# Kernel optimization log

Hardware: AMD Instinct MI355X
Metric: run time of the kernel (lower is better)

Reference implementation:

```python
import jax, jax.numpy as jnp
import numpy as np

N_NODES = 100000


def _gcn_norm(edge_index, edge_weight, n):
    # add self-loops with weight 1 (PyG gcn_norm default fill_value=1.0)
    row = jnp.concatenate([edge_index[0], jnp.arange(n, dtype=edge_index.dtype)])
    col = jnp.concatenate([edge_index[1], jnp.arange(n, dtype=edge_index.dtype)])
    w = jnp.concatenate([edge_weight, jnp.ones((n,), dtype=edge_weight.dtype)])
    deg = jax.ops.segment_sum(w, col, num_segments=n)
    dinv = jnp.where(deg > 0, jax.lax.rsqrt(jnp.where(deg > 0, deg, 1.0)), 0.0)
    norm = dinv[row] * w * dinv[col]  # [E+N]
    return row, col, norm


def _gcn_conv(x, row, col, norm, W, b, n):
    h = x @ W                                   # [N, out] dense projection first (in > out)
    msg = norm[:, None] * h[row]                # gather + scale
    out = jax.ops.segment_sum(msg, col, num_segments=n)  # scatter-add to targets
    return out + b


def setup_inputs() -> dict:
    key = jax.random.key(0)
    ks = jax.random.split(key, 6)
    n, e, f, h, c = N_NODES, 3200000, 256, 64, 40
    return {
        "x": jax.random.normal(ks[0], (n, f), dtype=jnp.float32),
        "edge_index": jax.random.randint(ks[1], (2, e), 0, n, dtype=jnp.int64),
        "edge_weight": jax.random.uniform(ks[2], (e,), dtype=jnp.float32),
        "W1": jax.random.normal(ks[3], (f, h), dtype=jnp.float32) / np.sqrt(f),
        "b1": jnp.zeros((h,), dtype=jnp.float32),
        "W2": jax.random.normal(ks[4], (h, c), dtype=jnp.float32) / np.sqrt(h),
        "b2": jnp.zeros((c,), dtype=jnp.float32),
    }


def reference(x, edge_index, edge_weight, W1, b1, W2, b2):
    n = x.shape[0]
    row, col, norm = _gcn_norm(edge_index, edge_weight, n)
    # layer 1: GCNConv -> identity activation -> dropout (identity at eval)
    h = _gcn_conv(x, row, col, norm, W1, b1, n)
    # layer 2: GCNConv (classifier head)
    out = _gcn_conv(h, row, col, norm, W2, b2, n)
    return out
```

## Files before the change

kernel.cpp:

```cpp
#include <hip/hip_runtime.h>
#include <hip/hip_fp16.h>
#include <cstdint>
#include <cstddef>


#define TB 256
#define NBK 200
#define LCAP 32
#define SPLIT 4
#define GCAP 2048
#define NSL 8

typedef _Float16 half8 __attribute__((ext_vector_type(8)));
typedef float f32x4 __attribute__((ext_vector_type(4)));

__global__ void k_detect(const unsigned* ei, int* flag) {
    int t = threadIdx.x;
    unsigned v = 0;
    for (int i = t; i < 256; i += 64) v |= ei[2 * i + 1];
    unsigned long long any = __ballot(v != 0u);
    if (t == 0) *flag = (any != 0ull) ? 1 : 0;
}

__global__ void k_zero(int* p, int n) {
    int i = blockIdx.x * blockDim.x + threadIdx.x;
    if (i < n) p[i] = 0;
}

__global__ __launch_bounds__(256) void k_binA(const void* __restrict__ ei,
                                              const int* __restrict__ flag,
                                              const float* __restrict__ ew,
                                              int* __restrict__ tail,
                                              int2* __restrict__ stage,
                                              int per, int E, int capx) {
    __shared__ int2 lbuf[NBK][LCAP];
    __shared__ int lcnt[NBK];
    int t = threadIdx.x;
    int myx = blockIdx.x & (NSL - 1);
    for (int i = t; i < NBK; i += 256) lcnt[i] = 0;
    __syncthreads();
    int s0 = blockIdx.x * per;
    int s1 = min(E, s0 + per);
    int isI32 = *flag;
    const int* p32 = (const int*)ei;
    const long long* p64 = (const long long*)ei;
    for (int b0 = s0; b0 < s1; b0 += 2048) {
        int2 ent[8];
        int bk[8];
#pragma unroll
        for (int u = 0; u < 8; u++) {
            int e = b0 + u * 256 + t;
            bk[u] = -1;
            if (e < s1) {
                int r, c;
                if (isI32) { r = p32[e]; c = p32[E + e]; }
                else       { r = (int)p64[e]; c = (int)p64[E + e]; }
                bk[u] = c >> 9;
                ent[u] = make_int2((r << 9) | (c & 511), __float_as_int(ew[e]));
            }
        }
#pragma unroll
        for (int u = 0; u < 8; u++) {
            if (bk[u] < 0) continue;
            int pos = atomicAdd(&lcnt[bk[u]], 1);
            if (pos < LCAP) {
                lbuf[bk[u]][pos] = ent[u];
            } else {
                int slot = bk[u] * NSL + myx;
                int g = atomicAdd(&tail[slot], 1);
                if (g < capx) stage[(size_t)slot * capx + g] = ent[u];
            }
        }
        __syncthreads();
        if (t < NBK) {
            int c = min(lcnt[t], LCAP);
            int n16 = c & ~15;
            if (n16) {
                int slot = t * NSL + myx;
                int base = atomicAdd(&tail[slot], n16);
                size_t db = (size_t)slot * capx;
                for (int j = 0; j < n16; j++) {
                    int g = base + j;
                    if (g < capx) stage[db + g] = lbuf[t][j];
                }
                int rem = c - n16;
                for (int j = 0; j < rem; j++) lbuf[t][j] = lbuf[t][n16 + j];
                lcnt[t] = rem;
            } else {
                lcnt[t] = c;
            }
        }
        __syncthreads();
    }
    if (t < NBK) {
        int c = min(lcnt[t], LCAP);
        if (c) {
            int slot = t * NSL + myx;
            int base = atomicAdd(&tail[slot], c);
            size_t db = (size_t)slot * capx;
            for (int j = 0; j < c; j++) {
                int g = base + j;
                if (g < capx) stage[db + g] = lbuf[t][j];
            }
        }
    }
}

__global__ void k_bscan(const int* __restrict__ tail, int* __restrict__ bbase,
                        int* __restrict__ ptr2, int nbk, int capx, int N) {
    __shared__ int sm[256];
    int t = threadIdx.x;
    int v = 0;
    if (t < nbk)
        for (int x = 0; x < NSL; x++) v += min(tail[t * NSL + x], capx);
    sm[t] = v;
    __syncthreads();
    for (int off = 1; off < 256; off <<= 1) {
        int add = (t >= off) ? sm[t - off] : 0;
        __syncthreads();
        sm[t] += add;
        __syncthreads();
    }
    if (t < nbk) bbase[t] = sm[t] - v;
    if (t == nbk - 1) ptr2[(size_t)N * 4] = sm[t];
}

__global__ __launch_bounds__(512) void k_binB(const int* __restrict__ tail,
                                              const int* __restrict__ bbase,
                                              const int2* __restrict__ stage,
                                              int2* __restrict__ csr,
                                              int* __restrict__ ptr2,
                                              float* __restrict__ dinv,
                                              int N, int capx, int qn) {
    __shared__ int h2[2048];
    __shared__ float wsm[512];
    __shared__ int sm[512];
    __shared__ int lpos2[2048];
    __shared__ int cseg[NSL];
    int b = blockIdx.x, t = threadIdx.x;
    for (int i = t; i < 2048; i += 512) h2[i] = 0;
    wsm[t] = 0.f;
    if (t < NSL) cseg[t] = min(tail[b * NSL + t], capx);
    __syncthreads();
#pragma unroll
    for (int x = 0; x < NSL; x++) {
        int m = cseg[x];
        size_t sb = (size_t)(b * NSL + x) * capx;
        for (int j = t; j < m; j += 512) {
            int2 v = stage[sb + j];
            int cl = v.x & 511;
            int src = v.x >> 9;
            int rng = min(src / qn, SPLIT - 1);
            atomicAdd(&h2[(cl << 2) | rng], 1);
            atomicAdd(&wsm[cl], __int_as_float(v.y));
        }
    }
    __syncthreads();
    int a0 = h2[t * 4], a1 = h2[t * 4 + 1], a2 = h2[t * 4 + 2], a3 = h2[t * 4 + 3];
    int s = a0 + a1 + a2 + a3;
    sm[t] = s;
    __syncthreads();
    for (int off = 1; off < 512; off <<= 1) {
        int add = (t >= off) ? sm[t - off] : 0;
        __syncthreads();
        sm[t] += add;
        __syncthreads();
    }
    int ex = sm[t] - s;
    int base = bbase[b];
    int node = b * 512 + t;
    int e0 = ex, e1 = ex + a0, e2 = e1 + a1, e3 = e2 + a2;
    float dv = rsqrtf(1.0f + wsm[t]);
    if (node < N) {
        ptr2[(size_t)node * 4 + 0] = base + e0;
        ptr2[(size_t)node * 4 + 1] = base + e1;
        ptr2[(size_t)node * 4 + 2] = base + e2;
        ptr2[(size_t)node * 4 + 3] = base + e3;
        dinv[node] = dv;
    }
    lpos2[t * 4 + 0] = e0;
    lpos2[t * 4 + 1] = e1;
    lpos2[t * 4 + 2] = e2;
    lpos2[t * 4 + 3] = e3;
    __syncthreads();
    wsm[t] = dv;
    __syncthreads();
#pragma unroll
    for (int x = 0; x < NSL; x++) {
        int m = cseg[x];
        size_t sb = (size_t)(b * NSL + x) * capx;
        for (int j = t; j < m; j += 512) {
            int2 v = stage[sb + j];
            int cl = v.x & 511;
            int src = v.x >> 9;
            int rng = min(src / qn, SPLIT - 1);
            int idx = atomicAdd(&lpos2[(cl << 2) | rng], 1);
            float wfold = __int_as_float(v.y) * wsm[cl];
            csr[base + idx] = make_int2(src, __float_as_int(wfold));
        }
    }
}

__global__ void k_fold(int2* __restrict__ csr, const float* __restrict__ dinv,
                       const int* __restrict__ ptr2, int n4) {
    int tot = ptr2[n4];
    int j = blockIdx.x * blockDim.x + threadIdx.x;
    if (j >= tot) return;
    int2 e = csr[j];
    csr[j].y = __float_as_int(__int_as_float(e.y) * dinv[e.x]);
}

__global__ void k_wc(const float* __restrict__ W1, const float* __restrict__ b1,
                     const float* __restrict__ W2, __half* __restrict__ Wcf,
                     float* __restrict__ bw) {
    __shared__ float w2s[64 * 40];
    __shared__ __half wcs[256][40];
    int t = threadIdx.x;
    for (int i = t; i < 64 * 40; i += 256) w2s[i] = W2[i];
    __syncthreads();
    float acc[40];
#pragma unroll
    for (int j = 0; j < 40; j++) acc[j] = 0.f;
    for (int k = 0; k < 64; k++) {
        float a = W1[t * 64 + k];
#pragma unroll
        for (int j = 0; j < 40; j++) acc[j] = fmaf(a, w2s[k * 40 + j], acc[j]);
    }
    for (int j = 0; j < 40; j++) wcs[t][j] = __float2half(acc[j]);
    if (t < 40) {
        float accb = 0.f;
        for (int k = 0; k < 64; k++) accb = fmaf(b1[k], w2s[k * 40 + t], accb);
        bw[t] = accb;
    }
    __syncthreads();
    for (int s = 0; s < 48; s++) {
        int o = t * 48 + s;
        int j = o & 7;
        int lane = (o >> 3) & 63;
        int f = o >> 9;
        int nt = f % 3, kt = f / 3;
        int k = kt * 32 + (lane >> 4) * 8 + j;
        int c = nt * 16 + (lane & 15);
        Wcf[o] = (c < 40) ? wcs[k][c] : __float2half(0.f);
    }
}

__global__ __launch_bounds__(256, 2) void k_zmm(const float* __restrict__ x,
                                                const __half* __restrict__ Wcf,
                                                __half* __restrict__ Zh, int n) {
    __shared__ __align__(16) unsigned char xs[128 * 64 * 2];
    int t = threadIdx.x;
    int w = t >> 6;
    int l = t & 63;
    int rlo = l & 15;
    int khi = l >> 4;
    int row0 = blockIdx.x * 128;
    f32x4 acc[2][3];
#pragma unroll
    for (int m = 0; m < 2; m++)
#pragma unroll
        for (int nt = 0; nt < 3; nt++) acc[m][nt] = (f32x4){0.f, 0.f, 0.f, 0.f};

    for (int k0 = 0; k0 < 256; k0 += 64) {
        __syncthreads();
#pragma unroll
        for (int s = 0; s < 8; s++) {
            int i = t + 256 * s;
            int rr = i >> 4;
            int kq = (i & 15) * 4;
            int grow = min(row0 + rr, n - 1);
            float4 v = *(const float4*)&x[(size_t)grow * 256 + k0 + kq];
            __half2 h01 = __floats2half2_rn(v.x, v.y);
            __half2 h23 = __floats2half2_rn(v.z, v.w);
            float2 pk;
            ((__half2*)&pk)[0] = h01;
            ((__half2*)&pk)[1] = h23;
            int byte = (rr * 128 + kq * 2) ^ ((rr & 7) << 4);
            *(float2*)(xs + byte) = pk;
        }
        __syncthreads();
        half8 bfr[2][3];
#pragma unroll
        for (int kt2 = 0; kt2 < 2; kt2++)
#pragma unroll
            for (int nt = 0; nt < 3; nt++) {
                int f = (k0 / 32 + kt2) * 3 + nt;
                bfr[kt2][nt] = *(const half8*)&Wcf[(size_t)(f * 64 + l) * 8];
            }
#pragma unroll
        for (int kt2 = 0; kt2 < 2; kt2++) {
#pragma unroll
            for (int m = 0; m < 2; m++) {
                int row = (w * 2 + m) * 16 + rlo;
                int byte = (row * 128 + kt2 * 64 + khi * 16) ^ ((row & 7) << 4);
                half8 af = *(const half8*)(xs + byte);
#pragma unroll
                for (int nt = 0; nt < 3; nt++)
                    acc[m][nt] = __builtin_amdgcn_mfma_f32_16x16x32_f16(af, bfr[kt2][nt], acc[m][nt], 0, 0, 0);
            }
        }
    }
#pragma unroll
    for (int m = 0; m < 2; m++) {
#pragma unroll
        for (int nt = 0; nt < 3; nt++) {
            int col = nt * 16 + rlo;
            if (col < 40) {
#pragma unroll
                for (int reg = 0; reg < 4; reg++) {
                    int grow = row0 + (w * 2 + m) * 16 + khi * 4 + reg;
                    if (grow < n) Zh[(size_t)grow * 40 + col] = __float2half(acc[m][nt][reg]);
                }
            }
        }
    }
}

template <int MODE>
__global__ __launch_bounds__(320) void k_gather(const int* __restrict__ ptr2,
                                                const int2* __restrict__ csr,
                                                const __half* __restrict__ src,
                                                const float* __restrict__ dinv,
                                                const float* __restrict__ bw,
                                                const float* __restrict__ b2,
                                                __half* __restrict__ dsth,
                                                float* __restrict__ dstf, int n) {
    __shared__ int2 se[GCAP];
    int t = threadIdx.x;
    int ln = t / 5;
    int q = t - ln * 5;
    int c0 = q * 8;
    int n0 = blockIdx.x * 64;
    int node = n0 + ln;
    int n1 = min(n0 + 64, n);
    int st0 = ptr2[(size_t)n0 * 4];
    int en0 = ptr2[(size_t)n1 * 4];
    bool act = (node < n1);
    float d2 = 0.f;
    int st = 0, en = 0;
    float a0 = 0.f, a1 = 0.f, a2 = 0.f, a3 = 0.f, a4 = 0.f, a5 = 0.f, a6 = 0.f, a7 = 0.f;
    float sw = 0.f;
    if (act) {
        float d = dinv[node];
        d2 = d * d;
        st = ptr2[(size_t)node * 4];
        en = ptr2[(size_t)(node + 1) * 4];
        float4 raw = *(const float4*)&src[(size_t)node * 40 + c0];
        const __half2* hh = (const __half2*)&raw;
        float2 f0 = __half22float2(hh[0]), f1 = __half22float2(hh[1]);
        float2 f2 = __half22float2(hh[2]), f3 = __half22float2(hh[3]);
        a0 = d2 * f0.x; a1 = d2 * f0.y; a2 = d2 * f1.x; a3 = d2 * f1.y;
        a4 = d2 * f2.x; a5 = d2 * f2.y; a6 = d2 * f3.x; a7 = d2 * f3.y;
    }
    for (int base = st0; base < en0; base += GCAP) {
        int m = min(GCAP, en0 - base);
        __syncthreads();
        for (int i = t; i < m; i += 320) se[i] = csr[base + i];
        __syncthreads();
        if (act) {
            int lo = max(st, base) - base;
            int hi = min(en, base + m) - base;
#pragma unroll 4
            for (int j = lo; j < hi; j++) {
                int2 e = se[j];
                float nv = __int_as_float(e.y);
                float4 raw = *(const float4*)&src[(size_t)e.x * 40 + c0];
                const __half2* hh = (const __half2*)&raw;
                float2 f0 = __half22float2(hh[0]), f1 = __half22float2(hh[1]);
                float2 f2 = __half22float2(hh[2]), f3 = __half22float2(hh[3]);
                if (MODE) sw += nv;
                a0 = fmaf(nv, f0.x, a0); a1 = fmaf(nv, f0.y, a1);
                a2 = fmaf(nv, f1.x, a2); a3 = fmaf(nv, f1.y, a3);
                a4 = fmaf(nv, f2.x, a4); a5 = fmaf(nv, f2.y, a5);
                a6 = fmaf(nv, f3.x, a6); a7 = fmaf(nv, f3.y, a7);
            }
        }
    }
    if (!act) return;
    if (MODE) {
        float sb = sw + d2;
        a0 += sb * bw[c0 + 0] + b2[c0 + 0];
        a1 += sb * bw[c0 + 1] + b2[c0 + 1];
        a2 += sb * bw[c0 + 2] + b2[c0 + 2];
        a3 += sb * bw[c0 + 3] + b2[c0 + 3];
        a4 += sb * bw[c0 + 4] + b2[c0 + 4];
        a5 += sb * bw[c0 + 5] + b2[c0 + 5];
        a6 += sb * bw[c0 + 6] + b2[c0 + 6];
        a7 += sb * bw[c0 + 7] + b2[c0 + 7];
        float4 o0 = make_float4(a0, a1, a2, a3);
        float4 o1 = make_float4(a4, a5, a6, a7);
        *(float4*)&dstf[(size_t)node * 40 + c0] = o0;
        *(float4*)&dstf[(size_t)node * 40 + c0 + 4] = o1;
    } else {
        float4 packed;
        ((__half2*)&packed)[0] = __floats2half2_rn(a0, a1);
        ((__half2*)&packed)[1] = __floats2half2_rn(a2, a3);
        ((__half2*)&packed)[2] = __floats2half2_rn(a4, a5);
        ((__half2*)&packed)[3] = __floats2half2_rn(a6, a7);
        *(float4*)&dsth[(size_t)node * 40 + c0] = packed;
    }
}

extern "C" void kernel_launch(void* const* d_in, const int* in_sizes, int n_in,
                              void* d_out, int out_size, void* d_ws, size_t ws_size,
                              hipStream_t stream) {
    const float* x  = (const float*)d_in[0];
    const void*  ei = d_in[1];
    const float* ew = (const float*)d_in[2];
    const float* W1 = (const float*)d_in[3];
    const float* b1 = (const float*)d_in[4];
    const float* W2 = (const float*)d_in[5];
    const float* b2 = (const float*)d_in[6];
    float* out = (float*)d_out;

    const int E = in_sizes[1] / 2;
    const int N = in_sizes[0] / 256;
    const int nbk = (N + 511) >> 9;
    const int capx = E / (nbk * NSL) + 768;
    const int qn = (N + SPLIT - 1) / SPLIT;

    char* ws = (char*)d_ws;
    float*  dinv = (float*)(ws + 0);
    int*    flag = (int*)(ws + (1u << 19));
    float*  bw   = (float*)(ws + (1u << 19) + 256);
    __half* Wcf  = (__half*)(ws + (1u << 19) + 4096);
    int*    tail = (int*)(ws + (1u << 19) + 65536);
    int*    bbase = (int*)(ws + (1u << 19) + 65536 + 16384);
    size_t off = (size_t)1 << 20;
    size_t estride = ((size_t)E * 4 + 255) & ~(size_t)255;
    size_t n4stride = ((size_t)(N * 4 + 1) * 4 + 255) & ~(size_t)255;
    size_t hstride = ((size_t)N * 40 * 2 + 255) & ~(size_t)255;
    int*    ptr2 = (int*)(ws + off);    off += n4stride;
    int2*   csr  = (int2*)(ws + off);   off += 2 * estride;
    int2*   stage = (int2*)(ws + off);  off += (size_t)NBK * NSL * capx * 8;
    __half* Zh   = (__half*)(ws + off); off += hstride;
    __half* T1h  = (__half*)(ws + off);

    const int NB = 608;
    const int per = (E + NB - 1) / NB;
    int gb = (N + 63) / 64;

    k_detect<<<1, 64, 0, stream>>>((const unsigned*)ei, flag);
    k_zero<<<(NBK * NSL + TB - 1) / TB, TB, 0, stream>>>(tail, NBK * NSL);
    k_binA<<<NB, 256, 0, stream>>>(ei, flag, ew, tail, stage, per, E, capx);
    k_bscan<<<1, 256, 0, stream>>>(tail, bbase, ptr2, nbk, capx, N);
    k_binB<<<nbk, 512, 0, stream>>>(tail, bbase, stage, csr, ptr2, dinv, N, capx, qn);
    k_fold<<<(E + TB - 1) / TB, TB, 0, stream>>>(csr, dinv, ptr2, N * 4);
    k_wc<<<1, TB, 0, stream>>>(W1, b1, W2, Wcf, bw);
    k_zmm<<<(N + 127) / 128, TB, 0, stream>>>(x, Wcf, Zh, N);
    k_gather<0><<<gb, 320, 0, stream>>>(ptr2, csr, Zh, dinv, bw, b2, T1h, nullptr, N);
    k_gather<1><<<gb, 320, 0, stream>>>(ptr2, csr, T1h, dinv, bw, b2, nullptr, out, N);
}
```

Baseline: 278.8 us.

## Split CSR binning into quarter-bucket blocks with LDS-staged coalesced writes

Each destination bucket of 512 nodes is now handled by four 256-thread blocks, one per 128-node quarter, which gives four times as many blocks for better GPU occupancy. Every block still scans the whole bucket's staged edges but only processes its own quarter. Per-quarter edge counts are reduced with wave shuffles to compute the output offset. Edges are scattered into an LDS buffer and then copied to the CSR array in coalesced order rather than scattered straight to global memory. The cost is reading the staged data four times, and edges beyond QCAP per quarter are silently dropped.

```diff
diff --git a/kernel.cpp b/kernel.cpp
--- a/kernel.cpp
+++ b/kernel.cpp
@@ -10,6 +10,7 @@
 #define SPLIT 4
 #define GCAP 2048
 #define NSL 8
+#define QCAP 5120
 
 typedef _Float16 half8 __attribute__((ext_vector_type(8)));
 typedef float f32x4 __attribute__((ext_vector_type(4)));
@@ -125,80 +126,106 @@
     if (t == nbk - 1) ptr2[(size_t)N * 4] = sm[t];
 }
 
-__global__ __launch_bounds__(512) void k_binB(const int* __restrict__ tail,
+__global__ __launch_bounds__(256) void k_binB(const int* __restrict__ tail,
                                               const int* __restrict__ bbase,
                                               const int2* __restrict__ stage,
                                               int2* __restrict__ csr,
                                               int* __restrict__ ptr2,
                                               float* __restrict__ dinv,
                                               int N, int capx, int qn) {
-    __shared__ int h2[2048];
-    __shared__ float wsm[512];
-    __shared__ int sm[512];
-    __shared__ int lpos2[2048];
+    __shared__ int2 lent[QCAP];
+    __shared__ int h2[512];
+    __shared__ int lpos[512];
+    __shared__ int sm[256];
+    __shared__ float wsm[128];
     __shared__ int cseg[NSL];
-    int b = blockIdx.x, t = threadIdx.x;
-    for (int i = t; i < 2048; i += 512) h2[i] = 0;
-    wsm[t] = 0.f;
+    __shared__ int qtot[4];
+    int b = blockIdx.x >> 2;
+    int qtr = blockIdx.x & 3;
+    int t = threadIdx.x;
+    for (int i = t; i < 512; i += 256) h2[i] = 0;
+    if (t < 128) wsm[t] = 0.f;
     if (t < NSL) cseg[t] = min(tail[b * NSL + t], capx);
-    __syncthreads();
-#pragma unroll
+    if (t < 4) qtot[t] = 0;
+    __syncthreads();
+    int cq0 = 0, cq1 = 0, cq2 = 0, cq3 = 0;
     for (int x = 0; x < NSL; x++) {
         int m = cseg[x];
         size_t sb = (size_t)(b * NSL + x) * capx;
-        for (int j = t; j < m; j += 512) {
+        for (int j = t; j < m; j += 256) {
             int2 v = stage[sb + j];
             int cl = v.x & 511;
-            int src = v.x >> 9;
-            int rng = min(src / qn, SPLIT - 1);
-            atomicAdd(&h2[(cl << 2) | rng], 1);
-            atomicAdd(&wsm[cl], __int_as_float(v.y));
-        }
-    }
-    __syncthreads();
-    int a0 = h2[t * 4], a1 = h2[t * 4 + 1], a2 = h2[t * 4 + 2], a3 = h2[t * 4 + 3];
-    int s = a0 + a1 + a2 + a3;
-    sm[t] = s;
-    __syncthreads();
-    for (int off = 1; off < 512; off <<= 1) {
+            int q = cl >> 7;
+            cq0 += (q == 0); cq1 += (q == 1); cq2 += (q == 2); cq3 += (q == 3);
+            if (q == qtr) {
+                int src = v.x >> 9;
+                int rng = min(src / qn, SPLIT - 1);
+                atomicAdd(&h2[((cl & 127) << 2) | rng], 1);
+                atomicAdd(&wsm[cl & 127], __int_as_float(v.y));
+            }
+        }
+    }
+#pragma unroll
+    for (int off = 32; off; off >>= 1) {
+        cq0 += __shfl_down(cq0, off);
+        cq1 += __shfl_down(cq1, off);
+        cq2 += __shfl_down(cq2, off);
+        cq3 += __shfl_down(cq3, off);
+    }
+    if ((t & 63) == 0) {
+        atomicAdd(&qtot[0], cq0);
+        atomicAdd(&qtot[1], cq1);
+        atomicAdd(&qtot[2], cq2);
+        atomicAdd(&qtot[3], cq3);
+    }
+    __syncthreads();
+    int p0 = h2[2 * t], p1 = h2[2 * t + 1];
+    int ps = p0 + p1;
+    sm[t] = ps;
+    __syncthreads();
+    for (int off = 1; off < 256; off <<= 1) {
         int add = (t >= off) ? sm[t - off] : 0;
         __syncthreads();
         sm[t] += add;
         __syncthreads();
     }
-    int ex = sm[t] - s;
-    int base = bbase[b];
-    int node = b * 512 + t;
-    int e0 = ex, e1 = ex + a0, e2 = e1 + a1, e3 = e2 + a2;
-    float dv = rsqrtf(1.0f + wsm[t]);
-    if (node < N) {
-        ptr2[(size_t)node * 4 + 0] = base + e0;
-        ptr2[(size_t)node * 4 + 1] = base + e1;
-        ptr2[(size_t)node * 4 + 2] = base + e2;
-        ptr2[(size_t)node * 4 + 3] = base + e3;
-        dinv[node] = dv;
-    }
-    lpos2[t * 4 + 0] = e0;
-    lpos2[t * 4 + 1] = e1;
-    lpos2[t * 4 + 2] = e2;
-    lpos2[t * 4 + 3] = e3;
-    __syncthreads();
-    wsm[t] = dv;
-    __syncthreads();
-#pragma unroll
+    int ex = sm[t] - ps;
+    int qb = bbase[b];
+    if (qtr > 0) qb += qtot[0];
+    if (qtr > 1) qb += qtot[1];
+    if (qtr > 2) qb += qtot[2];
+    lpos[2 * t] = ex;
+    lpos[2 * t + 1] = ex + p0;
+    int nodeBase = b * 512 + qtr * 128;
+    {
+        int k0 = 2 * t, k1 = 2 * t + 1;
+        int nl0 = nodeBase + (k0 >> 2), nl1 = nodeBase + (k1 >> 2);
+        if (nl0 < N) ptr2[(size_t)nl0 * 4 + (k0 & 3)] = qb + ex;
+        if (nl1 < N) ptr2[(size_t)nl1 * 4 + (k1 & 3)] = qb + ex + p0;
+    }
+    if (t < 128) {
+        float dv = rsqrtf(1.0f + wsm[t]);
+        if (nodeBase + t < N) dinv[nodeBase + t] = dv;
+        wsm[t] = dv;
+    }
+    __syncthreads();
     for (int x = 0; x < NSL; x++) {
         int m = cseg[x];
         size_t sb = (size_t)(b * NSL + x) * capx;
-        for (int j = t; j < m; j += 512) {
+        for (int j = t; j < m; j += 256) {
             int2 v = stage[sb + j];
             int cl = v.x & 511;
+            if ((cl >> 7) != qtr) continue;
             int src = v.x >> 9;
             int rng = min(src / qn, SPLIT - 1);
-            int idx = atomicAdd(&lpos2[(cl << 2) | rng], 1);
-            float wfold = __int_as_float(v.y) * wsm[cl];
-            csr[base + idx] = make_int2(src, __float_as_int(wfold));
-        }
-    }
+            int idx = atomicAdd(&lpos[((cl & 127) << 2) | rng], 1);
+            float wf = __int_as_float(v.y) * wsm[cl & 127];
+            if (idx < QCAP) lent[idx] = make_int2(src, __float_as_int(wf));
+        }
+    }
+    __syncthreads();
+    int tot = min(qtot[qtr], QCAP);
+    for (int i = t; i < tot; i += 256) csr[qb + i] = lent[i];
 }
 
 __global__ void k_fold(int2* __restrict__ csr, const float* __restrict__ dinv,
@@ -444,7 +471,7 @@
     k_zero<<<(NBK * NSL + TB - 1) / TB, TB, 0, stream>>>(tail, NBK * NSL);
     k_binA<<<NB, 256, 0, stream>>>(ei, flag, ew, tail, stage, per, E, capx);
     k_bscan<<<1, 256, 0, stream>>>(tail, bbase, ptr2, nbk, capx, N);
-    k_binB<<<nbk, 512, 0, stream>>>(tail, bbase, stage, csr, ptr2, dinv, N, capx, qn);
+    k_binB<<<nbk * 4, 256, 0, stream>>>(tail, bbase, stage, csr, ptr2, dinv, N, capx, qn);
     k_fold<<<(E + TB - 1) / TB, TB, 0, stream>>>(csr, dinv, ptr2, N * 4);
     k_wc<<<1, TB, 0, stream>>>(W1, b1, W2, Wcf, bw);
     k_zmm<<<(N + 127) / 128, TB, 0, stream>>>(x, Wcf, Zh, N);
```

After: 358.9 us. 28.7% more time.

## Stage CSR bucket writes in LDS per quarter for coalesced global stores

Applied to the files above, without the earlier changes.

Replaces k_binB's direct scattered global writes to csr with four passes, one per 128-node quarter of the bucket. Each pass builds its histogram and scan, scatters entries into a shared-memory buffer, and then copies that buffer to global memory contiguously. This targets the cost of random global stores, but the stage array is now read about nine times instead of twice. Any quarter holding more than QCAP entries would silently drop edges.

```diff
diff --git a/kernel.cpp b/kernel.cpp
--- a/kernel.cpp
+++ b/kernel.cpp
@@ -10,6 +10,7 @@
 #define SPLIT 4
 #define GCAP 2048
 #define NSL 8
+#define QCAP 5120
 
 typedef _Float16 half8 __attribute__((ext_vector_type(8)));
 typedef float f32x4 __attribute__((ext_vector_type(4)));
@@ -132,72 +133,85 @@
                                               int* __restrict__ ptr2,
                                               float* __restrict__ dinv,
                                               int N, int capx, int qn) {
-    __shared__ int h2[2048];
+    __shared__ int2 lent[QCAP];
+    __shared__ int h2[512];
+    __shared__ int lpos[512];
+    __shared__ int sm[512];
     __shared__ float wsm[512];
-    __shared__ int sm[512];
-    __shared__ int lpos2[2048];
     __shared__ int cseg[NSL];
+    __shared__ int qbase;
     int b = blockIdx.x, t = threadIdx.x;
-    for (int i = t; i < 2048; i += 512) h2[i] = 0;
     wsm[t] = 0.f;
     if (t < NSL) cseg[t] = min(tail[b * NSL + t], capx);
     __syncthreads();
-#pragma unroll
     for (int x = 0; x < NSL; x++) {
         int m = cseg[x];
         size_t sb = (size_t)(b * NSL + x) * capx;
         for (int j = t; j < m; j += 512) {
             int2 v = stage[sb + j];
-            int cl = v.x & 511;
-            int src = v.x >> 9;
-            int rng = min(src / qn, SPLIT - 1);
-            atomicAdd(&h2[(cl << 2) | rng], 1);
-            atomicAdd(&wsm[cl], __int_as_float(v.y));
-        }
-    }
-    __syncthreads();
-    int a0 = h2[t * 4], a1 = h2[t * 4 + 1], a2 = h2[t * 4 + 2], a3 = h2[t * 4 + 3];
-    int s = a0 + a1 + a2 + a3;
-    sm[t] = s;
-    __syncthreads();
-    for (int off = 1; off < 512; off <<= 1) {
-        int add = (t >= off) ? sm[t - off] : 0;
-        __syncthreads();
-        sm[t] += add;
-        __syncthreads();
-    }
-    int ex = sm[t] - s;
-    int base = bbase[b];
-    int node = b * 512 + t;
-    int e0 = ex, e1 = ex + a0, e2 = e1 + a1, e3 = e2 + a2;
+            atomicAdd(&wsm[v.x & 511], __int_as_float(v.y));
+        }
+    }
+    __syncthreads();
     float dv = rsqrtf(1.0f + wsm[t]);
-    if (node < N) {
-        ptr2[(size_t)node * 4 + 0] = base + e0;
-        ptr2[(size_t)node * 4 + 1] = base + e1;
-        ptr2[(size_t)node * 4 + 2] = base + e2;
-        ptr2[(size_t)node * 4 + 3] = base + e3;
-        dinv[node] = dv;
-    }
-    lpos2[t * 4 + 0] = e0;
-    lpos2[t * 4 + 1] = e1;
-    lpos2[t * 4 + 2] = e2;
-    lpos2[t * 4 + 3] = e3;
+    int node0 = b * 512 + t;
+    if (node0 < N) dinv[node0] = dv;
     __syncthreads();
     wsm[t] = dv;
-    __syncthreads();
-#pragma unroll
-    for (int x = 0; x < NSL; x++) {
-        int m = cseg[x];
-        size_t sb = (size_t)(b * NSL + x) * capx;
-        for (int j = t; j < m; j += 512) {
-            int2 v = stage[sb + j];
-            int cl = v.x & 511;
-            int src = v.x >> 9;
-            int rng = min(src / qn, SPLIT - 1);
-            int idx = atomicAdd(&lpos2[(cl << 2) | rng], 1);
-            float wfold = __int_as_float(v.y) * wsm[cl];
-            csr[base + idx] = make_int2(src, __float_as_int(wfold));
-        }
+    if (t == 0) qbase = bbase[b];
+    __syncthreads();
+    for (int qtr = 0; qtr < 4; qtr++) {
+        h2[t] = 0;
+        __syncthreads();
+        for (int x = 0; x < NSL; x++) {
+            int m = cseg[x];
+            size_t sb = (size_t)(b * NSL + x) * capx;
+            for (int j = t; j < m; j += 512) {
+                int2 v = stage[sb + j];
+                int cl = v.x & 511;
+                if ((cl >> 7) != qtr) continue;
+                int src = v.x >> 9;
+                int rng = min(src / qn, SPLIT - 1);
+                atomicAdd(&h2[((cl & 127) << 2) | rng], 1);
+            }
+        }
+        __syncthreads();
+        int hv = h2[t];
+        sm[t] = hv;
+        __syncthreads();
+        for (int off = 1; off < 512; off <<= 1) {
+            int add = (t >= off) ? sm[t - off] : 0;
+            __syncthreads();
+            sm[t] += add;
+            __syncthreads();
+        }
+        int ex = sm[t] - hv;
+        int qtot = sm[511];
+        int qb = qbase;
+        lpos[t] = ex;
+        int node = b * 512 + qtr * 128 + (t >> 2);
+        if (node < N) ptr2[(size_t)node * 4 + (t & 3)] = qb + ex;
+        __syncthreads();
+        for (int x = 0; x < NSL; x++) {
+            int m = cseg[x];
+            size_t sb = (size_t)(b * NSL + x) * capx;
+            for (int j = t; j < m; j += 512) {
+                int2 v = stage[sb + j];
+                int cl = v.x & 511;
+                if ((cl >> 7) != qtr) continue;
+                int src = v.x >> 9;
+                int rng = min(src / qn, SPLIT - 1);
+                int idx = atomicAdd(&lpos[((cl & 127) << 2) | rng], 1);
+                float wf = __int_as_float(v.y) * wsm[cl];
+                if (idx < QCAP) lent[idx] = make_int2(src, __float_as_int(wf));
+            }
+        }
+        __syncthreads();
+        int tot = min(qtot, QCAP);
+        for (int i = t; i < tot; i += 512) csr[qb + i] = lent[i];
+        __syncthreads();
+        if (t == 0) qbase = qb + qtot;
+        __syncthreads();
     }
 }
 
```

Measured after the change: 357.3 us. +28.2%, slower.
